# Optimization experiments

Measured on AMD Instinct MI355X. Metric: run time of the kernel, lower is better.

## Reference

```python
import jax, jax.numpy as jnp
import numpy as np

N_POINTS = 1_000_000
# Voigt index pairs (11,22,33,12,13,23)
_II = jnp.array([0, 1, 2, 0, 0, 1])
_JJ = jnp.array([0, 1, 2, 1, 2, 2])


def _P_of(F, c1, c2):
    """First Piola-Kirchhoff stress of compressible Neo-Hookean psi."""
    FinvT = jnp.linalg.inv(F).T
    I1 = jnp.trace(F.T @ F)
    J = jnp.linalg.det(F)
    Jm23 = jnp.power(J, -2.0 / 3.0)
    return 2.0 * c1 * Jm23 * (F - (I1 / 3.0) * FinvT) + 2.0 * c2 * (J - 1.0) * J * FinvT


def _per_point(F, c1, c2):
    I1 = jnp.trace(F.T @ F)
    J = jnp.linalg.det(F)
    Jm23 = jnp.power(J, -2.0 / 3.0)
    psi = c1 * (Jm23 * I1 - 3.0) + c2 * (J - 1.0) ** 2

    P = _P_of(F, c1, c2)                      # (3,3)
    P_F = jax.jacfwd(_P_of)(F, c1, c2)        # (3,3,3,3) = d P_ij / d F_kl

    Kirchhoff = P @ F.T                       # tau = P F^T
    Cauchy = Kirchhoff / J
    EYE = jnp.eye(3, dtype=F.dtype)

    # push-forward of the material tangent + geometric correction
    Stiff = jnp.einsum('iqks,jq,ls->ijkl', P_F, F, F)
    Stiff = Stiff + 0.5 * (
        jnp.einsum('ik,jl->ijkl', Kirchhoff, EYE)
        + jnp.einsum('il,jk->ijkl', Kirchhoff, EYE)
        + jnp.einsum('jk,il->ijkl', Kirchhoff, EYE)
        - jnp.einsum('jl,ik->ijkl', Kirchhoff, EYE)
    )

    Cauchy6 = Cauchy[_II, _JJ]                                            # (6,)
    DDSDDE = Stiff[_II[:, None], _JJ[:, None], _II[None, :], _JJ[None, :]] / J  # (6,6)
    return psi, Cauchy6, DDSDDE


def setup_inputs() -> dict:
    key = jax.random.key(0)
    k1, k2 = jax.random.split(key)
    # near-identity deformation gradients (positive det, small strain)
    noise = jax.random.normal(k1, (N_POINTS, 3, 3), dtype=jnp.float32)
    F_in = jnp.eye(3, dtype=jnp.float32)[None] + 0.05 * noise
    mat_par = 0.5 + jax.random.uniform(k2, (2,), dtype=jnp.float32)  # (c1, c2) > 0
    return {"F_in": F_in, "mat_par": mat_par}


def reference(F_in, mat_par):
    c1, c2 = mat_par[0], mat_par[1]
    psi, Cauchy6, DDSDDE = jax.vmap(_per_point, in_axes=(0, None, None))(F_in, c1, c2)
    return psi, Cauchy6, DDSDDE
```

## Files before the change

kernel.cpp:

```cpp
#include <hip/hip_runtime.h>

static constexpr int VII[6] = {0, 1, 2, 0, 0, 1};
static constexpr int VJJ[6] = {0, 1, 2, 1, 2, 2};

template <bool VEC>
__global__ __launch_bounds__(256) void nh3d_kernel(
    const float* __restrict__ Fg, const float* __restrict__ mp,
    float* __restrict__ out, int N)
{
    const int idx = blockIdx.x * blockDim.x + threadIdx.x;
    if (idx >= N) return;

    const float c1 = mp[0];
    const float c2 = mp[1];

    float F[3][3];
    {
        const float* fp = Fg + (size_t)idx * 9;
#pragma unroll
        for (int r = 0; r < 3; ++r)
#pragma unroll
            for (int c = 0; c < 3; ++c)
                F[r][c] = fp[3 * r + c];
    }

    const float J = F[0][0] * (F[1][1] * F[2][2] - F[1][2] * F[2][1])
                  - F[0][1] * (F[1][0] * F[2][2] - F[1][2] * F[2][0])
                  + F[0][2] * (F[1][0] * F[2][1] - F[1][1] * F[2][0]);

    float b[3][3];
#pragma unroll
    for (int r = 0; r < 3; ++r)
#pragma unroll
        for (int c = 0; c < 3; ++c) {
            if (c > r) continue;
            const float s = F[r][0] * F[c][0] + F[r][1] * F[c][1] + F[r][2] * F[c][2];
            b[r][c] = s;
            b[c][r] = s;
        }

    const float I1   = b[0][0] + b[1][1] + b[2][2];
    const float invJ = 1.0f / J;
    const float Jm23 = cbrtf(invJ * invJ);

    const float psi = c1 * (Jm23 * I1 - 3.0f) + c2 * (J - 1.0f) * (J - 1.0f);

    const float c1t  = 2.0f * c1 * Jm23;
    const float diag = 2.0f * c2 * (J - 1.0f) * J - c1t * (I1 * (1.0f / 3.0f));
    float tau[3][3];
#pragma unroll
    for (int r = 0; r < 3; ++r)
#pragma unroll
        for (int c = 0; c < 3; ++c)
            tau[r][c] = c1t * b[r][c] + (r == c ? diag : 0.0f);

    float cau[6];
#pragma unroll
    for (int a = 0; a < 6; ++a)
        cau[a] = tau[VII[a]][VJJ[a]] * invJ;

    const float gE  = 2.0f * c2 * (2.0f * J - 1.0f) * J;
    const float gF  = -2.0f * c2 * (J - 1.0f) * J;
    const float cA  = c1t * (2.0f * I1 * (1.0f / 9.0f));
    const float cB  = c1t * (I1 * (1.0f / 3.0f));
    const float m23 = -(2.0f / 3.0f) * c1t;

    float dd[36];
#pragma unroll
    for (int a = 0; a < 6; ++a) {
        const int i = VII[a], j = VJJ[a];
#pragma unroll
        for (int q = 0; q < 6; ++q) {
            const int k = VII[q], l = VJJ[q];
            float s = 0.0f;
            if (i == k) s += c1t * b[j][l];
            if (k == l) s += m23 * b[i][j];
            if (i == j) s += m23 * b[k][l];
            if (i == j && k == l) s += cA + gE;
            if (i == l && j == k) s += cB + gF;
            float g = 0.0f;
            if (j == l) g += tau[i][k];
            if (j == k) g += tau[i][l];
            if (i == l) g += tau[j][k];
            if (i == k) g -= tau[j][l];
            dd[6 * a + q] = (s + 0.5f * g) * invJ;
        }
    }

    out[idx] = psi;
    float* cout_ = out + (size_t)N + (size_t)idx * 6;
    float* dout_ = out + (size_t)7 * N + (size_t)idx * 36;
    if (VEC) {
#pragma unroll
        for (int v = 0; v < 3; ++v)
            *reinterpret_cast<float2*>(cout_ + 2 * v) =
                make_float2(cau[2 * v], cau[2 * v + 1]);
#pragma unroll
        for (int v = 0; v < 9; ++v)
            *reinterpret_cast<float4*>(dout_ + 4 * v) =
                make_float4(dd[4 * v], dd[4 * v + 1], dd[4 * v + 2], dd[4 * v + 3]);
    } else {
#pragma unroll
        for (int a = 0; a < 6; ++a) cout_[a] = cau[a];
#pragma unroll
        for (int a = 0; a < 36; ++a) dout_[a] = dd[a];
    }
}

extern "C" void kernel_launch(void* const* d_in, const int* in_sizes, int n_in,
                              void* d_out, int out_size, void* d_ws, size_t ws_size,
                              hipStream_t stream) {
    const int N = in_sizes[0] / 9;
    const float* F_in    = (const float*)d_in[0];
    const float* mat_par = (const float*)d_in[1];
    float* out = (float*)d_out;

    const int block = 256;
    const int grid  = (N + block - 1) / block;

    if (N % 4 == 0) {
        nh3d_kernel<true><<<grid, block, 0, stream>>>(F_in, mat_par, out, N);
    } else {
        nh3d_kernel<false><<<grid, block, 0, stream>>>(F_in, mat_par, out, N);
    }
}
```

Before: 217.4 us.

## Stage per-wave outputs through LDS to coalesce global stores

Each wave writes its 36-entry tangent and 6-entry stress results into padded shared memory, then reads them back so consecutive lanes emit contiguous float4/float2 global stores. This replaces per-thread strided stores, which touch many cache lines per instruction. A scalar fallback kernel handles the tail and unaligned sizes. The change costs about 37 KB of LDS per block, which may reduce occupancy, and adds LDS traffic with possible bank conflicts.

```diff
diff --git a/kernel.cpp b/kernel.cpp
--- a/kernel.cpp
+++ b/kernel.cpp
@@ -3,27 +3,9 @@
 static constexpr int VII[6] = {0, 1, 2, 0, 0, 1};
 static constexpr int VJJ[6] = {0, 1, 2, 1, 2, 2};
 
-template <bool VEC>
-__global__ __launch_bounds__(256) void nh3d_kernel(
-    const float* __restrict__ Fg, const float* __restrict__ mp,
-    float* __restrict__ out, int N)
+__device__ __forceinline__ void nh_compute(const float F[3][3], float c1, float c2,
+                                           float& psi, float cau[6], float dd[36])
 {
-    const int idx = blockIdx.x * blockDim.x + threadIdx.x;
-    if (idx >= N) return;
-
-    const float c1 = mp[0];
-    const float c2 = mp[1];
-
-    float F[3][3];
-    {
-        const float* fp = Fg + (size_t)idx * 9;
-#pragma unroll
-        for (int r = 0; r < 3; ++r)
-#pragma unroll
-            for (int c = 0; c < 3; ++c)
-                F[r][c] = fp[3 * r + c];
-    }
-
     const float J = F[0][0] * (F[1][1] * F[2][2] - F[1][2] * F[2][1])
                   - F[0][1] * (F[1][0] * F[2][2] - F[1][2] * F[2][0])
                   + F[0][2] * (F[1][0] * F[2][1] - F[1][1] * F[2][0]);
@@ -43,7 +25,7 @@
     const float invJ = 1.0f / J;
     const float Jm23 = cbrtf(invJ * invJ);
 
-    const float psi = c1 * (Jm23 * I1 - 3.0f) + c2 * (J - 1.0f) * (J - 1.0f);
+    psi = c1 * (Jm23 * I1 - 3.0f) + c2 * (J - 1.0f) * (J - 1.0f);
 
     const float c1t  = 2.0f * c1 * Jm23;
     const float diag = 2.0f * c2 * (J - 1.0f) * J - c1t * (I1 * (1.0f / 3.0f));
@@ -54,7 +36,6 @@
         for (int c = 0; c < 3; ++c)
             tau[r][c] = c1t * b[r][c] + (r == c ? diag : 0.0f);
 
-    float cau[6];
 #pragma unroll
     for (int a = 0; a < 6; ++a)
         cau[a] = tau[VII[a]][VJJ[a]] * invJ;
@@ -65,7 +46,6 @@
     const float cB  = c1t * (I1 * (1.0f / 3.0f));
     const float m23 = -(2.0f / 3.0f) * c1t;
 
-    float dd[36];
 #pragma unroll
     for (int a = 0; a < 6; ++a) {
         const int i = VII[a], j = VJJ[a];
@@ -86,25 +66,103 @@
             dd[6 * a + q] = (s + 0.5f * g) * invJ;
         }
     }
+}
+
+#define WPB 4
+#define DPAD 37
+
+__global__ __launch_bounds__(256) void nh3d_coal(
+    const float* __restrict__ Fg, const float* __restrict__ mp,
+    float* __restrict__ out, int N, int nWaves)
+{
+    __shared__ float sbuf[WPB][64 * DPAD];
+
+    const int tid  = threadIdx.x;
+    const int wave = tid >> 6;
+    const int lane = tid & 63;
+    const int waveIdx = blockIdx.x * WPB + wave;
+    if (waveIdx >= nWaves) return;
+    const int waveStart = waveIdx * 64;
+    const int idx = waveStart + lane;
+
+    const float c1 = mp[0];
+    const float c2 = mp[1];
+
+    float F[3][3];
+    {
+        const float* fp = Fg + (size_t)idx * 9;
+#pragma unroll
+        for (int r = 0; r < 3; ++r)
+#pragma unroll
+            for (int c = 0; c < 3; ++c)
+                F[r][c] = fp[3 * r + c];
+    }
+
+    float psi, cau[6], dd[36];
+    nh_compute(F, c1, c2, psi, cau, dd);
+
+    out[idx] = psi;
+
+    float* sw = sbuf[wave];
+
+#pragma unroll
+    for (int j = 0; j < 36; ++j)
+        sw[lane * DPAD + j] = dd[j];
+
+    float* dout = out + (size_t)7 * N + (size_t)waveStart * 36;
+#pragma unroll
+    for (int k = 0; k < 9; ++k) {
+        const int g = k * 256 + lane * 4;
+        const int p = g / 36;
+        const int base = p * DPAD + (g - p * 36);
+        const float4 v = make_float4(sw[base], sw[base + 1], sw[base + 2], sw[base + 3]);
+        *reinterpret_cast<float4*>(dout + g) = v;
+    }
+
+#pragma unroll
+    for (int j = 0; j < 6; ++j)
+        sw[lane * 7 + j] = cau[j];
+
+    float* cout_ = out + (size_t)N + (size_t)waveStart * 6;
+#pragma unroll
+    for (int k = 0; k < 3; ++k) {
+        const int g = k * 128 + lane * 2;
+        const int p = g / 6;
+        const int base = p * 7 + (g - p * 6);
+        *reinterpret_cast<float2*>(cout_ + g) = make_float2(sw[base], sw[base + 1]);
+    }
+}
+
+__global__ __launch_bounds__(256) void nh3d_scatter(
+    const float* __restrict__ Fg, const float* __restrict__ mp,
+    float* __restrict__ out, int N, int start)
+{
+    const int idx = start + blockIdx.x * blockDim.x + threadIdx.x;
+    if (idx >= N) return;
+
+    const float c1 = mp[0];
+    const float c2 = mp[1];
+
+    float F[3][3];
+    {
+        const float* fp = Fg + (size_t)idx * 9;
+#pragma unroll
+        for (int r = 0; r < 3; ++r)
+#pragma unroll
+            for (int c = 0; c < 3; ++c)
+                F[r][c] = fp[3 * r + c];
+    }
+
+    float psi, cau[6], dd[36];
+    nh_compute(F, c1, c2, psi, cau, dd);
 
     out[idx] = psi;
     float* cout_ = out + (size_t)N + (size_t)idx * 6;
-    float* dout_ = out + (size_t)7 * N + (size_t)idx * 36;
-    if (VEC) {
+    float* dout  = out + (size_t)7 * N + (size_t)idx * 36;
 #pragma unroll
-        for (int v = 0; v < 3; ++v)
-            *reinterpret_cast<float2*>(cout_ + 2 * v) =
-                make_float2(cau[2 * v], cau[2 * v + 1]);
+    for (int a = 0; a < 6; ++a) cout_[a] = cau[a];
 #pragma unroll
-        for (int v = 0; v < 9; ++v)
-            *reinterpret_cast<float4*>(dout_ + 4 * v) =
-                make_float4(dd[4 * v], dd[4 * v + 1], dd[4 * v + 2], dd[4 * v + 3]);
-    } else {
-#pragma unroll
-        for (int a = 0; a < 6; ++a) cout_[a] = cau[a];
-#pragma unroll
-        for (int a = 0; a < 36; ++a) dout_[a] = dd[a];
-    }
+    for (int a = 0; a < 36; ++a) dout[a] = dd[a];
 }
 
 extern "C" void kernel_launch(void* const* d_in, const int* in_sizes, int n_in,
@@ -115,12 +173,16 @@
     const float* mat_par = (const float*)d_in[1];
     float* out = (float*)d_out;
 
-    const int block = 256;
-    const int grid  = (N + block - 1) / block;
-
-    if (N % 4 == 0) {
-        nh3d_kernel<true><<<grid, block, 0, stream>>>(F_in, mat_par, out, N);
+    if (N >= 64 && (N % 4) == 0) {
+        const int nWaves = N / 64;
+        const int grid = (nWaves + WPB - 1) / WPB;
+        nh3d_coal<<<grid, 256, 0, stream>>>(F_in, mat_par, out, N, nWaves);
+        const int tail = N - nWaves * 64;
+        if (tail > 0) {
+            nh3d_scatter<<<1, 64, 0, stream>>>(F_in, mat_par, out, N, nWaves * 64);
+        }
     } else {
-        nh3d_kernel<false><<<grid, block, 0, stream>>>(F_in, mat_par, out, N);
+        const int grid = (N + 255) / 256;
+        nh3d_scatter<<<grid, 256, 0, stream>>>(F_in, mat_par, out, N, 0);
     }
 }
```

Result: faster. 194.0 us (-10.8%).
